# Performance work log

Measured on AMD Instinct MI355X. Metric: run time of the kernel, lower is better.

Reference implementation:

```python
import jax, jax.numpy as jnp
import numpy as np

NUM_USER = 24000
NUM_ITEM = 8000
DIM_E = 64
V_DIM = 2048
T_DIM = 384
TOPK = 10
N_UI_LAYERS = 2
LAMBDA = 0.9
N_INTER = 400000


def _build_sim(x):
    xn = x / jnp.linalg.norm(x, axis=-1, keepdims=True)
    return xn @ xn.T


def _knn_sym(sim, topk):
    # top-k per row -> sparse graph with symmetric (D^-1/2 A D^-1/2) normalization
    n = sim.shape[0]
    val, ind = jax.lax.top_k(sim, topk)            # [n, k]
    row = jnp.repeat(jnp.arange(n), topk)
    w = val.reshape(-1)
    col = ind.reshape(-1)
    deg = jax.ops.segment_sum(w, row, num_segments=n)
    dis = jnp.where(deg > 0, deg ** -0.5, 0.0)     # inf -> 0 as in torch masked_fill
    return col, dis[row] * w * dis[col]


def setup_inputs() -> dict:
    key = jax.random.key(0)
    ks = jax.random.split(key, 12)
    user_emb = jax.random.normal(ks[0], (NUM_USER, DIM_E), jnp.float32) * 0.1
    item_emb = jax.random.normal(ks[1], (NUM_ITEM, DIM_E), jnp.float32) * 0.1
    v_feat = jax.random.normal(ks[2], (NUM_ITEM, V_DIM), jnp.float32)
    t_feat = jax.random.normal(ks[3], (NUM_ITEM, T_DIM), jnp.float32)
    W_v = jax.random.normal(ks[4], (V_DIM, DIM_E), jnp.float32) * (1.0 / np.sqrt(V_DIM))
    b_v = jnp.zeros((DIM_E,), jnp.float32)
    W_t = jax.random.normal(ks[5], (T_DIM, DIM_E), jnp.float32) * (1.0 / np.sqrt(T_DIM))
    b_t = jnp.zeros((DIM_E,), jnp.float32)
    Wq1 = jax.random.normal(ks[6], (DIM_E, DIM_E), jnp.float32) * (1.0 / np.sqrt(DIM_E))
    bq1 = jnp.zeros((DIM_E,), jnp.float32)
    wq2 = jax.random.normal(ks[7], (DIM_E,), jnp.float32) * (1.0 / np.sqrt(DIM_E))
    # bipartite user-item interaction edges, symmetrized (as in __init__)
    u = jax.random.randint(ks[8], (N_INTER,), 0, NUM_USER)
    it = jax.random.randint(ks[9], (N_INTER,), 0, NUM_ITEM) + NUM_USER
    ei = jnp.stack([u, it])
    edge_index = jnp.concatenate([ei, ei[::-1]], axis=1)  # [2, 2*N_INTER]
    # original (frozen) multimodal KNN graphs built from raw features at init
    orig_img_cols, orig_img_w = _knn_sym(_build_sim(v_feat), TOPK)
    orig_txt_cols, orig_txt_w = _knn_sym(_build_sim(t_feat), TOPK)
    return {"user_emb": user_emb, "item_emb": item_emb, "v_feat": v_feat,
            "t_feat": t_feat, "W_v": W_v, "b_v": b_v, "W_t": W_t, "b_t": b_t,
            "Wq1": Wq1, "bq1": bq1, "wq2": wq2,
            "orig_img_w": orig_img_w, "orig_txt_w": orig_txt_w,
            "edge_index": edge_index,
            "orig_img_cols": orig_img_cols, "orig_txt_cols": orig_txt_cols}


def reference(user_emb, item_emb, v_feat, t_feat, W_v, b_v, W_t, b_t,
              Wq1, bq1, wq2, orig_img_w, orig_txt_w,
              edge_index, orig_img_cols, orig_txt_cols):
    n_user, n_item = user_emb.shape[0], item_emb.shape[0]
    # modality projections
    image_feats = v_feat @ W_v + b_v
    text_feats = t_feat @ W_t + b_t
    # fresh KNN graphs from projected features (build_item_graph=True path)
    img_cols, img_w = _knn_sym(_build_sim(image_feats), TOPK)
    txt_cols, txt_w = _knn_sym(_build_sim(text_feats), TOPK)
    row = jnp.repeat(jnp.arange(n_item), TOPK)

    def fused_spmm(cols_new, w_new, cols_orig, w_orig, x):
        # (1-lam)*A_new + lam*A_orig, applied as a single sparse matmul
        rows = jnp.concatenate([row, row])
        cols = jnp.concatenate([cols_new, cols_orig])
        w = jnp.concatenate([(1.0 - LAMBDA) * w_new,
                             LAMBDA * jax.lax.stop_gradient(w_orig)])
        return jax.ops.segment_sum(w[:, None] * x[cols], rows, num_segments=n_item)

    # NOTE: source bug reproduced - mm_layers loop always re-reads item_embedding,
    # so effective propagation depth is 1 regardless of mm_layers.
    image_item = fused_spmm(img_cols, img_w, orig_img_cols, orig_img_w, item_emb)
    text_item = fused_spmm(txt_cols, txt_w, orig_txt_cols, orig_txt_w, item_emb)

    def q(x):
        return jnp.tanh(x @ Wq1 + bq1) @ wq2  # [n_item]

    att = jnp.stack([q(image_item), q(text_item)], axis=-1)  # [n_item, 2]
    wgt = jax.nn.softmax(att, axis=-1)
    h = wgt[:, :1] * image_item + wgt[:, 1:] * text_item

    # user-item GCN propagation with sym degree normalization
    ego = jnp.concatenate([user_emb, item_emb], axis=0)
    n = ego.shape[0]
    r, c = edge_index[0], edge_index[1]
    deg = jax.ops.segment_sum(jnp.ones_like(r, dtype=ego.dtype), r, num_segments=n)
    dis = jnp.where(deg > 0, deg ** -0.5, 0.0)
    norm = dis[r] * dis[c]
    embs = [ego]
    for _ in range(N_UI_LAYERS):
        ego = jax.ops.segment_sum(norm[:, None] * ego[c], r, num_segments=n)
        embs.append(ego)
    all_emb = jnp.mean(jnp.stack(embs, axis=1), axis=1)
    u_g, i_g = all_emb[:n_user], all_emb[n_user:]
    h_norm = h / jnp.maximum(jnp.linalg.norm(h, axis=1, keepdims=True), 1e-12)
    i_g = i_g + h_norm
    return jnp.concatenate([u_g, i_g], axis=0)
```

## Files before the change

### kernel.cpp

```cpp
#include <hip/hip_runtime.h>
#include <math.h>

#define N_USER 24000
#define N_ITEM 8000
#define N_NODE 32000
#define N_EDGE 800000
#define NJC    16
#define JCH    512

typedef __attribute__((ext_vector_type(8))) short bf16x8;
typedef __attribute__((ext_vector_type(4))) float f32x4;

__device__ __forceinline__ float wred_sum(float v) {
#pragma unroll
  for (int off = 32; off; off >>= 1) v += __shfl_xor(v, off, 64);
  return v;
}

__device__ __forceinline__ unsigned short f2bf(float f) {
  unsigned int u = __float_as_uint(f);
  unsigned int r = (u + 0x7fffu + ((u >> 16) & 1u)) >> 16;
  return (unsigned short)r;
}
__device__ __forceinline__ float bf2f(unsigned short h) {
  return __uint_as_float(((unsigned int)h) << 16);
}

__device__ __forceinline__ unsigned int umx(unsigned int a, unsigned int b) { return a > b ? a : b; }
__device__ __forceinline__ unsigned int umn(unsigned int a, unsigned int b) { return a < b ? a : b; }
__device__ __forceinline__ unsigned int umed3(unsigned int a, unsigned int b, unsigned int c) {
  unsigned int d;
  asm("v_med3_u32 %0, %1, %2, %3" : "=v"(d) : "v"(a), "v"(b), "v"(c));
  return d;
}

__device__ __forceinline__ float key_val(unsigned int k) {
  return ((float)(int)(k >> 13) - 131080.0f) * (1.0f / 131072.0f);
}
__device__ __forceinline__ int key_idx(unsigned int k) {
  return 8191 - (int)(k & 8191u);
}

#define NB_G 378
__global__ __launch_bounds__(256) void k_gemm_count(
    const float* __restrict__ Xi, const float* __restrict__ Wi,
    const float* __restrict__ Xt, const float* __restrict__ Wt,
    float* __restrict__ Pi, float* __restrict__ Pt,
    const int* __restrict__ r, int* __restrict__ degi)
{
  __shared__ char lds2[24576];
  char* ldsXH = lds2;
  char* ldsXL = lds2 + 8192;
  char* ldsWH = lds2 + 16384;
  char* ldsWL = lds2 + 20480;
  const int tid = threadIdx.x;
  const int b = blockIdx.x;
  if (b >= NB_G) {
    int e = (b - NB_G) * 256 + tid;
    atomicAdd(&degi[r[e]], 1);
    return;
  }
  const int m0 = (b % 63) * 128;
  const int cy = b / 63;
  const float* X; const float* W; float* out; int K, kc0, ksteps;
  if (cy < 4) { X = Xi; W = Wi; K = 2048; kc0 = cy * 512; ksteps = 16;
                out = Pi + (size_t)cy * N_ITEM * 64; }
  else        { X = Xt; W = Wt; K = 384;  kc0 = (cy - 4) * 192; ksteps = 6;
                out = Pt + (size_t)(cy - 4) * N_ITEM * 64; }
  const int l = tid & 63;
  const int wid = tid >> 6;
  f32x4 acc[2][4] = {};

  for (int ks = 0; ks < ksteps; ++ks) {
    int k0 = kc0 + ks * 32;
    __syncthreads();
#pragma unroll
    for (int lq = 0; lq < 4; ++lq) {
      int u = tid + lq * 256;
      int rr = u >> 3, q = u & 7;
      int grow = m0 + rr; if (grow > N_ITEM - 1) grow = N_ITEM - 1;
      float4 xv = *(const float4*)(X + (size_t)grow * K + k0 + q * 4);
      unsigned short h0 = f2bf(xv.x), h1 = f2bf(xv.y), h2 = f2bf(xv.z), h3 = f2bf(xv.w);
      unsigned int hA = ((unsigned int)h1 << 16) | h0;
      unsigned int hB = ((unsigned int)h3 << 16) | h2;
      unsigned short l0 = f2bf(xv.x - bf2f(h0)), l1 = f2bf(xv.y - bf2f(h1));
      unsigned short l2 = f2bf(xv.z - bf2f(h2)), l3 = f2bf(xv.w - bf2f(h3));
      unsigned int lA = ((unsigned int)l1 << 16) | l0;
      unsigned int lB = ((unsigned int)l3 << 16) | l2;
      int slot = q >> 1;
      int bo = rr * 64 + ((slot ^ ((rr >> 1) & 3)) << 4) + (q & 1) * 8;
      *(int2*)(ldsXH + bo) = make_int2((int)hA, (int)hB);
      *(int2*)(ldsXL + bo) = make_int2((int)lA, (int)lB);
    }
#pragma unroll
    for (int lq = 0; lq < 2; ++lq) {
      int u = tid + lq * 256;
      int kb = u >> 4, nq = (u & 15) * 4;
      float4 wv = *(const float4*)(W + (size_t)(k0 + kb) * 64 + nq);
      int slot = kb >> 3, within = kb & 7;
      float wa[4] = {wv.x, wv.y, wv.z, wv.w};
#pragma unroll
      for (int j = 0; j < 4; ++j) {
        int n = nq + j;
        unsigned short h = f2bf(wa[j]);
        unsigned short lo = f2bf(wa[j] - bf2f(h));
        int bo = n * 64 + ((slot ^ ((n >> 1) & 3)) << 4) + within * 2;
        *(unsigned short*)(ldsWH + bo) = h;
        *(unsigned short*)(ldsWL + bo) = lo;
      }
    }
    __syncthreads();
    bf16x8 xh[2], xl[2], wh[4], wl[4];
    int slot = l >> 4;
#pragma unroll
    for (int s = 0; s < 2; ++s) {
      int rr = wid * 32 + s * 16 + (l & 15);
      int bo = rr * 64 + ((slot ^ ((rr >> 1) & 3)) << 4);
      xh[s] = *(const bf16x8*)(ldsXH + bo);
      xl[s] = *(const bf16x8*)(ldsXL + bo);
    }
#pragma unroll
    for (int nt = 0; nt < 4; ++nt) {
      int n = nt * 16 + (l & 15);
      int bo = n * 64 + ((slot ^ ((n >> 1) & 3)) << 4);
      wh[nt] = *(const bf16x8*)(ldsWH + bo);
      wl[nt] = *(const bf16x8*)(ldsWL + bo);
    }
#pragma unroll
    for (int s = 0; s < 2; ++s)
#pragma unroll
      for (int nt = 0; nt < 4; ++nt) {
        acc[s][nt] = __builtin_amdgcn_mfma_f32_16x16x32_bf16(xh[s], wh[nt], acc[s][nt], 0, 0, 0);
        acc[s][nt] = __builtin_amdgcn_mfma_f32_16x16x32_bf16(xh[s], wl[nt], acc[s][nt], 0, 0, 0);
        acc[s][nt] = __builtin_amdgcn_mfma_f32_16x16x32_bf16(xl[s], wh[nt], acc[s][nt], 0, 0, 0);
      }
  }
#pragma unroll
  for (int s = 0; s < 2; ++s)
#pragma unroll
    for (int nt = 0; nt < 4; ++nt)
#pragma unroll
      for (int r4 = 0; r4 < 4; ++r4) {
        int gi = m0 + wid * 32 + s * 16 + ((l >> 4) << 2) + r4;
        int gn = nt * 16 + (l & 15);
        if (gi < N_ITEM) out[(size_t)gi * 64 + gn] = acc[s][nt][r4];
      }
}

__global__ __launch_bounds__(256) void norm_dual(
    const float* __restrict__ Pi, const float* __restrict__ bi,
    unsigned short* __restrict__ Xhi, unsigned short* __restrict__ Xli,
    const float* __restrict__ Pt, const float* __restrict__ bt,
    unsigned short* __restrict__ Xht, unsigned short* __restrict__ Xlt)
{
  const float* P; const float* bias; unsigned short *Xh, *Xl; int nk;
  if (blockIdx.y == 0) { P = Pi; bias = bi; Xh = Xhi; Xl = Xli; nk = 4; }
  else                 { P = Pt; bias = bt; Xh = Xht; Xl = Xlt; nk = 2; }
  int row = blockIdx.x * 4 + (threadIdx.x >> 6);
  int lane = threadIdx.x & 63;
  size_t o = (size_t)row * 64 + lane;
  float v = bias[lane];
  for (int q = 0; q < nk; ++q) v += P[(size_t)q * N_ITEM * 64 + o];
  float ss = wred_sum(v * v);
  float xn = v * rsqrtf(ss);
  unsigned short hi = f2bf(xn);
  Xh[o] = hi;
  Xl[o] = f2bf(xn - bf2f(hi));
}

#define NB_SIM 2016
__global__ __launch_bounds__(256) void k_sim_scan(
    const unsigned short* __restrict__ Xhi, const unsigned short* __restrict__ Xli,
    const unsigned short* __restrict__ Xht, const unsigned short* __restrict__ Xlt,
    unsigned int* __restrict__ pk,
    const int* __restrict__ degi, int* __restrict__ offs, float* __restrict__ disui)
{
  __shared__ char lds[2 * 2 * 32 * 128];
  const int tid = threadIdx.x;

  if (blockIdx.x == 0) {
    int* stot  = (int*)lds;
    int* sbase = (int*)lds + 512;
    int lane = tid & 63, w = tid >> 6;
    for (int k = 0; k < 125; ++k) {
      int c = w * 125 + k;
      int d = degi[c * 64 + lane];
      int s = d;
#pragma unroll
      for (int off = 32; off; off >>= 1) s += __shfl_xor(s, off, 64);
      if (lane == 0) stot[c] = s;
    }
    __syncthreads();
    if (w == 0) {
      int run = 0;
      for (int r = 0; r < 8; ++r) {
        int idx = r * 64 + lane;
        int v = (idx < 500) ? stot[idx] : 0;
        int p = v;
#pragma unroll
        for (int off = 1; off < 64; off <<= 1) {
          int n = __shfl_up(p, off, 64);
          if (lane >= off) p += n;
        }
        if (idx < 500) sbase[idx] = run + p - v;
        run += __shfl(p, 63, 64);
      }
    }
    __syncthreads();
    for (int k = 0; k < 125; ++k) {
      int c = w * 125 + k;
      int i = c * 64 + lane;
      int d = degi[i];
      int p = d;
#pragma unroll
      for (int off = 1; off < 64; off <<= 1) {
        int n = __shfl_up(p, off, 64);
        if (lane >= off) p += n;
      }
      offs[i] = sbase[c] + p - d;
      disui[i] = d > 0 ? rsqrtf((float)d) : 0.f;
    }
    if (tid == 0) offs[N_NODE] = N_EDGE;
    return;
  }

  const int b = blockIdx.x - 1;
  const int bz = b / 1008;
  const int rem = b % 1008;
  const int by = rem / 63;
  const int bx = rem % 63;
  const unsigned short* Xh = bz ? Xht : Xhi;
  const unsigned short* Xl = bz ? Xlt : Xli;
  unsigned int* pkm = pk + (size_t)bz * N_ITEM * (NJC * 10);

  const int l = tid & 63;
  const int wid = tid >> 6;
  const int ib = bx * 128 + wid * 32;
  const int jc = by * JCH;
  const bool lastc = (jc + JCH > N_ITEM);

  bf16x8 bh[2][2], bl[2][2];
#pragma unroll
  for (int s = 0; s < 2; ++s) {
    int irow = ib + s * 16 + (l & 15);
    if (irow > N_ITEM - 1) irow = N_ITEM - 1;
    int ksl = (l >> 4) * 8;
#pragma unroll
    for (int kh = 0; kh < 2; ++kh) {
      bh[s][kh] = *(const bf16x8*)(Xh + (size_t)irow * 64 + kh * 32 + ksl);
      bl[s][kh] = *(const bf16x8*)(Xl + (size_t)irow * 64 + kh * 32 + ksl);
    }
  }

  unsigned int K0[10], K1[10];
#pragma unroll
  for (int t = 0; t < 10; ++t) { K0[t] = 0u; K1[t] = 0u; }

  auto stage = [&](int bb, int p) {
    int row = tid >> 3, cb = (tid & 7) * 16;
    int gr = jc + p * 32 + row;
    if (gr > N_ITEM - 1) gr = N_ITEM - 1;
    int4 vh = *(const int4*)(Xh + (size_t)gr * 64 + (cb >> 1));
    int4 vl = *(const int4*)(Xl + (size_t)gr * 64 + (cb >> 1));
    int bo = (row * 128 + cb) ^ ((row & 7) << 4);
    *(int4*)(lds + bb * 8192 + bo) = vh;
    *(int4*)(lds + bb * 8192 + 4096 + bo) = vl;
  };

#define EPI(MASKED)                                                            \
  _Pragma("unroll")                                                            \
  for (int s = 0; s < 2; ++s) {                                                \
    unsigned int* K = s ? K1 : K0;                                             \
    _Pragma("unroll")                                                          \
    for (int t = 0; t < 2; ++t) {                                              \
      _Pragma("unroll")                                                        \
      for (int r = 0; r < 4; ++r) {                                            \
        float f = acc[t][s][r];                                                \
        unsigned int v19 = (unsigned int)(int)(f * 131072.0f + 131080.0f);     \
        unsigned int key = (v19 << 13) | (unsigned int)jinv[t * 4 + r];        \
        if (MASKED) key = (jinv[t * 4 + r] >= 192) ? key : 0u;                 \
        _Pragma("unroll")                                                      \
        for (int q = 9; q >= 1; --q) K[q] = umed3(K[q - 1], K[q], key);        \
        K[0] = umx(K[0], key);                                                 \
      }                                                                        \
    }                                                                          \
  }

  stage(0, 0);
  int cur = 0;
  for (int p = 0; p < 16; ++p) {
    __syncthreads();
    if (p < 15) stage(cur ^ 1, p + 1);
    const char* ldsH = lds + cur * 8192;
    const char* ldsL = ldsH + 4096;
    f32x4 acc[2][2] = {};
#pragma unroll
    for (int t = 0; t < 2; ++t) {
      int jr = t * 16 + (l & 15);
      int sw = (jr & 7) << 4;
      int rb = jr * 128 + ((l >> 4) << 4);
      bf16x8 ah0 = *(const bf16x8*)(ldsH + (rb ^ sw));
      bf16x8 ah1 = *(const bf16x8*)(ldsH + ((rb + 64) ^ sw));
      bf16x8 al0 = *(const bf16x8*)(ldsL + (rb ^ sw));
      bf16x8 al1 = *(const bf16x8*)(ldsL + ((rb + 64) ^ sw));
#pragma unroll
      for (int s = 0; s < 2; ++s) {
        acc[t][s] = __builtin_amdgcn_mfma_f32_16x16x32_bf16(ah0, bh[s][0], acc[t][s], 0, 0, 0);
        acc[t][s] = __builtin_amdgcn_mfma_f32_16x16x32_bf16(ah1, bh[s][1], acc[t][s], 0, 0, 0);
        acc[t][s] = __builtin_amdgcn_mfma_f32_16x16x32_bf16(ah0, bl[s][0], acc[t][s], 0, 0, 0);
        acc[t][s] = __builtin_amdgcn_mfma_f32_16x16x32_bf16(ah1, bl[s][1], acc[t][s], 0, 0, 0);
        acc[t][s] = __builtin_amdgcn_mfma_f32_16x16x32_bf16(al0, bh[s][0], acc[t][s], 0, 0, 0);
        acc[t][s] = __builtin_amdgcn_mfma_f32_16x16x32_bf16(al1, bh[s][1], acc[t][s], 0, 0, 0);
      }
    }
    const int jg0 = jc + p * 32 + ((l >> 4) << 2);
    int jinv[8];
#pragma unroll
    for (int t = 0; t < 2; ++t)
#pragma unroll
      for (int r = 0; r < 4; ++r)
        jinv[t * 4 + r] = 8191 - (jg0 + t * 16 + r);
    if (!lastc) { EPI(false) } else { EPI(true) }
    cur ^= 1;
  }
#undef EPI

#pragma unroll
  for (int s = 0; s < 2; ++s) {
    unsigned int* K = s ? K1 : K0;
    unsigned int kv[10];
#pragma unroll
    for (int t = 0; t < 10; ++t) {
      unsigned int m = K[0];
      m = umx(m, (unsigned int)__shfl_xor((int)m, 16, 64));
      m = umx(m, (unsigned int)__shfl_xor((int)m, 32, 64));
      bool own = (K[0] == m);
#pragma unroll
      for (int q2 = 0; q2 < 9; ++q2) K[q2] = own ? K[q2 + 1] : K[q2];
      K[9] = own ? 0u : K[9];
      kv[t] = m;
    }
    int i = ib + s * 16 + (l & 15);
    if (l < 16 && i < N_ITEM) {
      size_t base = ((size_t)i * NJC + by) * 10;
#pragma unroll
      for (int t = 0; t < 10; ++t) pkm[base + t] = kv[t];
    }
  }
}

#define NB_M 4000
__global__ __launch_bounds__(256) void k_merge_fill(
    const unsigned int* __restrict__ pk,
    float* __restrict__ tv_i, int* __restrict__ tc_i, float* __restrict__ dis_i,
    float* __restrict__ tv_t, int* __restrict__ tc_t, float* __restrict__ dis_t,
    const int* __restrict__ r, const int* __restrict__ c,
    const int* __restrict__ offs, int* __restrict__ cursor, int* __restrict__ csr)
{
  int b = blockIdx.x;
  int tid = threadIdx.x;
  if (b >= NB_M) {
    int e = (b - NB_M) * 256 + tid;
    int rr = r[e];
    int pos = offs[rr] + atomicAdd(&cursor[rr], 1);
    csr[pos] = c[e];
    return;
  }
  int my = b / 2000, mx = b % 2000;
  float* tv; int* tc; float* dis;
  if (my == 0) { tv = tv_i; tc = tc_i; dis = dis_i; }
  else         { tv = tv_t; tc = tc_t; dis = dis_t; }
  int lane = tid & 63;
  int row = mx * 4 + (tid >> 6);
  size_t base = (size_t)my * N_ITEM * (NJC * 10) + (size_t)row * (NJC * 10);
  unsigned int k0 = pk[base + lane];
  unsigned int k1 = pk[base + 64 + lane];
  unsigned int k2 = (lane < 32) ? pk[base + 128 + lane] : 0u;
  float deg = 0.f, keepv = 0.f; int keepc = 0;
  for (int t = 0; t < 10; ++t) {
    unsigned int m = umx(umx(k0, k1), k2);
#pragma unroll
    for (int off = 32; off; off >>= 1)
      m = umx(m, (unsigned int)__shfl_xor((int)m, off, 64));
    deg += key_val(m);
    if (k0 == m) k0 = 0u;
    else if (k1 == m) k1 = 0u;
    else if (k2 == m) k2 = 0u;
    if (lane == t) { keepv = key_val(m); keepc = key_idx(m); }
  }
  if (lane < 10) { tv[(size_t)row * 10 + lane] = keepv; tc[(size_t)row * 10 + lane] = keepc; }
  if (lane == 0) dis[row] = deg > 0.f ? rsqrtf(deg) : 0.f;
}

#define NB_S 2000
__global__ __launch_bounds__(256) void k_spmm_prop1(
    const float* __restrict__ tv_i, const int* __restrict__ tc_i, const float* __restrict__ dis_i,
    const float* __restrict__ ow_i, const int* __restrict__ oc_i,
    const float* __restrict__ tv_t, const int* __restrict__ tc_t, const float* __restrict__ dis_t,
    const float* __restrict__ ow_t, const int* __restrict__ oc_t,
    const float* __restrict__ item_emb,
    const float* __restrict__ Wq1, const float* __restrict__ bq1,
    const float* __restrict__ wq2, float* __restrict__ hn,
    const float* __restrict__ ue, float* __restrict__ E1,
    const int* __restrict__ offs, const int* __restrict__ csr,
    const float* __restrict__ dis)
{
  __shared__ float Wlds[64 * 64];
  __shared__ float sm[4][2][64];
  int tid = threadIdx.x;
  int lane = tid & 63, wid = tid >> 6;
  int b = blockIdx.x;
  if (b >= NB_S) {
    int row = (b - NB_S) * 4 + wid;
    int q = lane >> 3, c8 = lane & 7;
    float4 acc0 = make_float4(0.f, 0.f, 0.f, 0.f);
    float4 acc1 = make_float4(0.f, 0.f, 0.f, 0.f);
    int e0 = offs[row], e1 = offs[row + 1];
    for (int e = e0 + q; e < e1; e += 8) {
      int cc = csr[e];
      const float* src = cc < N_USER ? ue + (size_t)cc * 64
                                     : item_emb + (size_t)(cc - N_USER) * 64;
      float4 v0 = *(const float4*)(src + c8 * 8);
      float4 v1 = *(const float4*)(src + c8 * 8 + 4);
      float d = dis[cc];
      acc0.x += d * v0.x; acc0.y += d * v0.y; acc0.z += d * v0.z; acc0.w += d * v0.w;
      acc1.x += d * v1.x; acc1.y += d * v1.y; acc1.z += d * v1.z; acc1.w += d * v1.w;
    }
#pragma unroll
    for (int off = 8; off <= 32; off <<= 1) {
      acc0.x += __shfl_xor(acc0.x, off, 64);
      acc0.y += __shfl_xor(acc0.y, off, 64);
      acc0.z += __shfl_xor(acc0.z, off, 64);
      acc0.w += __shfl_xor(acc0.w, off, 64);
      acc1.x += __shfl_xor(acc1.x, off, 64);
      acc1.y += __shfl_xor(acc1.y, off, 64);
      acc1.z += __shfl_xor(acc1.z, off, 64);
      acc1.w += __shfl_xor(acc1.w, off, 64);
    }
    if (q == 0) {
      float dr = dis[row];
      acc0.x *= dr; acc0.y *= dr; acc0.z *= dr; acc0.w *= dr;
      acc1.x *= dr; acc1.y *= dr; acc1.z *= dr; acc1.w *= dr;
      *(float4*)(E1 + (size_t)row * 64 + c8 * 8) = acc0;
      *(float4*)(E1 + (size_t)row * 64 + c8 * 8 + 4) = acc1;
    }
    return;
  }
  int row = b * 4 + wid;
#pragma unroll
  for (int s = 0; s < 4; ++s) {
    int idx = tid + s * 256;
    ((float4*)Wlds)[idx] = ((const float4*)Wq1)[idx];
  }
  float a0 = 0.f, a1 = 0.f;
  {
    float disr = dis_i[row];
#pragma unroll
    for (int t = 0; t < 10; ++t) {
      int c = tc_i[(size_t)row * 10 + t];
      a0 += 0.1f * disr * tv_i[(size_t)row * 10 + t] * dis_i[c] * item_emb[(size_t)c * 64 + lane];
    }
#pragma unroll
    for (int t = 0; t < 10; ++t) {
      int c = oc_i[(size_t)row * 10 + t];
      a0 += 0.9f * ow_i[(size_t)row * 10 + t] * item_emb[(size_t)c * 64 + lane];
    }
  }
  {
    float disr = dis_t[row];
#pragma unroll
    for (int t = 0; t < 10; ++t) {
      int c = tc_t[(size_t)row * 10 + t];
      a1 += 0.1f * disr * tv_t[(size_t)row * 10 + t] * dis_t[c] * item_emb[(size_t)c * 64 + lane];
    }
#pragma unroll
    for (int t = 0; t < 10; ++t) {
      int c = oc_t[(size_t)row * 10 + t];
      a1 += 0.9f * ow_t[(size_t)row * 10 + t] * item_emb[(size_t)c * 64 + lane];
    }
  }
  sm[wid][0][lane] = a0;
  sm[wid][1][lane] = a1;
  __syncthreads();
  float y0 = bq1[lane], y1 = bq1[lane];
  for (int k = 0; k < 64; ++k) {
    float w = Wlds[k * 64 + lane];
    y0 += sm[wid][0][k] * w;
    y1 += sm[wid][1][k] * w;
  }
  float wq = wq2[lane];
  float s0 = wred_sum(tanhf(y0) * wq);
  float s1 = wred_sum(tanhf(y1) * wq);
  float mx = fmaxf(s0, s1);
  float e0 = expf(s0 - mx), e1 = expf(s1 - mx);
  float inv = 1.f / (e0 + e1);
  float h = (e0 * inv) * a0 + (e1 * inv) * a1;
  float n2 = wred_sum(h * h);
  float nrm = fmaxf(sqrtf(n2), 1e-12f);
  hn[(size_t)row * 64 + lane] = h / nrm;
}

__global__ __launch_bounds__(256) void k_prop2(
    const float* __restrict__ in, const float* __restrict__ ue,
    const float* __restrict__ ie, float* __restrict__ out,
    const int* __restrict__ offs, const int* __restrict__ csr,
    const float* __restrict__ dis, const float* __restrict__ hn)
{
  int tid = threadIdx.x;
  int lane = tid & 63, wid = tid >> 6;
  int row = blockIdx.x * 4 + wid;
  int q = lane >> 3, c8 = lane & 7;
  float4 acc0 = make_float4(0.f, 0.f, 0.f, 0.f);
  float4 acc1 = make_float4(0.f, 0.f, 0.f, 0.f);
  int e0 = offs[row], e1 = offs[row + 1];
  for (int e = e0 + q; e < e1; e += 8) {
    int cc = csr[e];
    const float* src = in + (size_t)cc * 64;
    float4 v0 = *(const float4*)(src + c8 * 8);
    float4 v1 = *(const float4*)(src + c8 * 8 + 4);
    float d = dis[cc];
    acc0.x += d * v0.x; acc0.y += d * v0.y; acc0.z += d * v0.z; acc0.w += d * v0.w;
    acc1.x += d * v1.x; acc1.y += d * v1.y; acc1.z += d * v1.z; acc1.w += d * v1.w;
  }
#pragma unroll
  for (int off = 8; off <= 32; off <<= 1) {
    acc0.x += __shfl_xor(acc0.x, off, 64);
    acc0.y += __shfl_xor(acc0.y, off, 64);
    acc0.z += __shfl_xor(acc0.z, off, 64);
    acc0.w += __shfl_xor(acc0.w, off, 64);
    acc1.x += __shfl_xor(acc1.x, off, 64);
    acc1.y += __shfl_xor(acc1.y, off, 64);
    acc1.z += __shfl_xor(acc1.z, off, 64);
    acc1.w += __shfl_xor(acc1.w, off, 64);
  }
  if (q == 0) {
    float dr = dis[row];
    acc0.x *= dr; acc0.y *= dr; acc0.z *= dr; acc0.w *= dr;
    acc1.x *= dr; acc1.y *= dr; acc1.z *= dr; acc1.w *= dr;
    const float* egop = (row < N_USER) ? ue + (size_t)row * 64
                                       : ie + (size_t)(row - N_USER) * 64;
    float4 eg0 = *(const float4*)(egop + c8 * 8);
    float4 eg1 = *(const float4*)(egop + c8 * 8 + 4);
    float4 l10 = *(const float4*)(in + (size_t)row * 64 + c8 * 8);
    float4 l11 = *(const float4*)(in + (size_t)row * 64 + c8 * 8 + 4);
    float4 o0, o1;
    o0.x = (eg0.x + l10.x + acc0.x) * (1.f / 3.f);
    o0.y = (eg0.y + l10.y + acc0.y) * (1.f / 3.f);
    o0.z = (eg0.z + l10.z + acc0.z) * (1.f / 3.f);
    o0.w = (eg0.w + l10.w + acc0.w) * (1.f / 3.f);
    o1.x = (eg1.x + l11.x + acc1.x) * (1.f / 3.f);
    o1.y = (eg1.y + l11.y + acc1.y) * (1.f / 3.f);
    o1.z = (eg1.z + l11.z + acc1.z) * (1.f / 3.f);
    o1.w = (eg1.w + l11.w + acc1.w) * (1.f / 3.f);
    if (row >= N_USER) {
      const float* hp = hn + (size_t)(row - N_USER) * 64;
      float4 h0 = *(const float4*)(hp + c8 * 8);
      float4 h1 = *(const float4*)(hp + c8 * 8 + 4);
      o0.x += h0.x; o0.y += h0.y; o0.z += h0.z; o0.w += h0.w;
      o1.x += h1.x; o1.y += h1.y; o1.z += h1.z; o1.w += h1.w;
    }
    *(float4*)(out + (size_t)row * 64 + c8 * 8) = o0;
    *(float4*)(out + (size_t)row * 64 + c8 * 8 + 4) = o1;
  }
}

extern "C" void kernel_launch(void* const* d_in, const int* in_sizes, int n_in,
                              void* d_out, int out_size, void* d_ws, size_t ws_size,
                              hipStream_t stream)
{
  (void)in_sizes; (void)n_in; (void)out_size; (void)ws_size;
  const float* user_emb = (const float*)d_in[0];
  const float* item_emb = (const float*)d_in[1];
  const float* v_feat   = (const float*)d_in[2];
  const float* t_feat   = (const float*)d_in[3];
  const float* W_v      = (const float*)d_in[4];
  const float* b_v      = (const float*)d_in[5];
  const float* W_t      = (const float*)d_in[6];
  const float* b_t      = (const float*)d_in[7];
  const float* Wq1      = (const float*)d_in[8];
  const float* bq1      = (const float*)d_in[9];
  const float* wq2      = (const float*)d_in[10];
  const float* ow_i     = (const float*)d_in[11];
  const float* ow_t     = (const float*)d_in[12];
  const int*   eidx     = (const int*)d_in[13];
  const int*   oc_i     = (const int*)d_in[14];
  const int*   oc_t     = (const int*)d_in[15];
  float* out = (float*)d_out;

  char* wp = (char*)d_ws;
  auto alloc = [&](size_t bytes) -> void* {
    void* p = (void*)wp;
    wp += (bytes + 255) & ~(size_t)255;
    return p;
  };
  char* regionA = (char*)alloc((size_t)8 * N_ITEM * 64 * 4 + 1024);
  char* regionB = (char*)alloc((size_t)N_NODE * 64 * 4 + 1024);
  float* Pp_i = (float*)regionA;
  float* Pp_t = (float*)regionB;
  unsigned int* pk = (unsigned int*)regionA;
  float* E1 = (float*)regionB;

  unsigned short* Xhi = (unsigned short*)alloc((size_t)N_ITEM * 64 * 2);
  unsigned short* Xli = (unsigned short*)alloc((size_t)N_ITEM * 64 * 2);
  unsigned short* Xht = (unsigned short*)alloc((size_t)N_ITEM * 64 * 2);
  unsigned short* Xlt = (unsigned short*)alloc((size_t)N_ITEM * 64 * 2);
  float* tv_i  = (float*)alloc((size_t)N_ITEM * 10 * 4);
  int*   tc_i  = (int*)  alloc((size_t)N_ITEM * 10 * 4);
  float* dis_i = (float*)alloc((size_t)N_ITEM * 4);
  float* tv_t  = (float*)alloc((size_t)N_ITEM * 10 * 4);
  int*   tc_t  = (int*)  alloc((size_t)N_ITEM * 10 * 4);
  float* dis_t = (float*)alloc((size_t)N_ITEM * 4);
  float* hn    = (float*)alloc((size_t)N_ITEM * 64 * 4);
  int*   degcur= (int*)  alloc((size_t)2 * N_NODE * 4);
  int*   degi  = degcur;
  int*   curs  = degcur + N_NODE;
  int*   offs  = (int*)  alloc((size_t)(N_NODE + 1) * 4);
  float* disui = (float*)alloc((size_t)N_NODE * 4);
  int*   csr   = (int*)  alloc((size_t)N_EDGE * 4);

  hipMemsetAsync(degcur, 0, (size_t)2 * N_NODE * 4, stream);
  k_gemm_count<<<NB_G + 3125, 256, 0, stream>>>(v_feat, W_v, t_feat, W_t, Pp_i, Pp_t,
                                                eidx, degi);
  norm_dual<<<dim3(2000, 2), 256, 0, stream>>>(Pp_i, b_v, Xhi, Xli, Pp_t, b_t, Xht, Xlt);
  k_sim_scan<<<NB_SIM + 1, 256, 0, stream>>>(Xhi, Xli, Xht, Xlt, pk, degi, offs, disui);
  k_merge_fill<<<NB_M + 3125, 256, 0, stream>>>(pk, tv_i, tc_i, dis_i, tv_t, tc_t, dis_t,
                                                eidx, eidx + N_EDGE, offs, curs, csr);
  k_spmm_prop1<<<NB_S + 8000, 256, 0, stream>>>(tv_i, tc_i, dis_i, ow_i, oc_i,
                                                tv_t, tc_t, dis_t, ow_t, oc_t,
                                                item_emb, Wq1, bq1, wq2, hn,
                                                user_emb, E1, offs, csr, disui);
  k_prop2<<<8000, 256, 0, stream>>>(E1, user_emb, item_emb, out, offs, csr, disui, hn);
}
```

Measured before the change: 301.0 us.

## Double similarity-scan block size so each staged column tile serves more rows

The similarity top-k kernel moves from 256 to 512 threads per block, with each block covering 256 item rows instead of 128. The grid shrinks from 2016 to 1024 scan blocks, and each thread stages half as many bytes (int2 instead of int4) into the shared LDS tile. The aim is to reuse each staged column chunk across twice as many rows, cutting redundant global loads of the column features. The trade-offs are fewer blocks for occupancy, 8-byte LDS writes, and a rebalanced prefix-scan block, which now uses 8 waves with bounds checks.

Result: no change. 305.3 us (+1.4%).

```diff
diff --git a/kernel.cpp b/kernel.cpp
--- a/kernel.cpp
+++ b/kernel.cpp
@@ -168,8 +168,8 @@
   Xl[o] = f2bf(xn - bf2f(hi));
 }
 
-#define NB_SIM 2016
-__global__ __launch_bounds__(256) void k_sim_scan(
+#define NB_SIM 1024
+__global__ __launch_bounds__(512) void k_sim_scan(
     const unsigned short* __restrict__ Xhi, const unsigned short* __restrict__ Xli,
     const unsigned short* __restrict__ Xht, const unsigned short* __restrict__ Xlt,
     unsigned int* __restrict__ pk,
@@ -177,65 +177,68 @@
 {
   __shared__ char lds[2 * 2 * 32 * 128];
   const int tid = threadIdx.x;
+  const int l = tid & 63;
+  const int wid = tid >> 6;
 
   if (blockIdx.x == 0) {
     int* stot  = (int*)lds;
     int* sbase = (int*)lds + 512;
-    int lane = tid & 63, w = tid >> 6;
-    for (int k = 0; k < 125; ++k) {
-      int c = w * 125 + k;
-      int d = degi[c * 64 + lane];
-      int s = d;
-#pragma unroll
-      for (int off = 32; off; off >>= 1) s += __shfl_xor(s, off, 64);
-      if (lane == 0) stot[c] = s;
+    for (int k = 0; k < 63; ++k) {
+      int c = wid * 63 + k;
+      if (c < 500) {
+        int d = degi[c * 64 + l];
+        int s = d;
+#pragma unroll
+        for (int off = 32; off; off >>= 1) s += __shfl_xor(s, off, 64);
+        if (l == 0) stot[c] = s;
+      }
     }
     __syncthreads();
-    if (w == 0) {
+    if (wid == 0) {
       int run = 0;
       for (int r = 0; r < 8; ++r) {
-        int idx = r * 64 + lane;
+        int idx = r * 64 + l;
         int v = (idx < 500) ? stot[idx] : 0;
         int p = v;
 #pragma unroll
         for (int off = 1; off < 64; off <<= 1) {
           int n = __shfl_up(p, off, 64);
-          if (lane >= off) p += n;
+          if (l >= off) p += n;
         }
         if (idx < 500) sbase[idx] = run + p - v;
         run += __shfl(p, 63, 64);
       }
     }
     __syncthreads();
-    for (int k = 0; k < 125; ++k) {
-      int c = w * 125 + k;
-      int i = c * 64 + lane;
-      int d = degi[i];
-      int p = d;
-#pragma unroll
-      for (int off = 1; off < 64; off <<= 1) {
-        int n = __shfl_up(p, off, 64);
-        if (lane >= off) p += n;
+    for (int k = 0; k < 63; ++k) {
+      int c = wid * 63 + k;
+      if (c < 500) {
+        int i = c * 64 + l;
+        int d = degi[i];
+        int p = d;
+#pragma unroll
+        for (int off = 1; off < 64; off <<= 1) {
+          int n = __shfl_up(p, off, 64);
+          if (l >= off) p += n;
+        }
+        offs[i] = sbase[c] + p - d;
+        disui[i] = d > 0 ? rsqrtf((float)d) : 0.f;
       }
-      offs[i] = sbase[c] + p - d;
-      disui[i] = d > 0 ? rsqrtf((float)d) : 0.f;
     }
     if (tid == 0) offs[N_NODE] = N_EDGE;
     return;
   }
 
   const int b = blockIdx.x - 1;
-  const int bz = b / 1008;
-  const int rem = b % 1008;
-  const int by = rem / 63;
-  const int bx = rem % 63;
+  const int bz = b >> 9;
+  const int rem = b & 511;
+  const int by = rem >> 5;
+  const int bx = rem & 31;
   const unsigned short* Xh = bz ? Xht : Xhi;
   const unsigned short* Xl = bz ? Xlt : Xli;
   unsigned int* pkm = pk + (size_t)bz * N_ITEM * (NJC * 10);
 
-  const int l = tid & 63;
-  const int wid = tid >> 6;
-  const int ib = bx * 128 + wid * 32;
+  const int ib = bx * 256 + wid * 32;
   const int jc = by * JCH;
   const bool lastc = (jc + JCH > N_ITEM);
 
@@ -257,14 +260,14 @@
   for (int t = 0; t < 10; ++t) { K0[t] = 0u; K1[t] = 0u; }
 
   auto stage = [&](int bb, int p) {
-    int row = tid >> 3, cb = (tid & 7) * 16;
+    int row = tid >> 4, cb = (tid & 15) * 8;
     int gr = jc + p * 32 + row;
     if (gr > N_ITEM - 1) gr = N_ITEM - 1;
-    int4 vh = *(const int4*)(Xh + (size_t)gr * 64 + (cb >> 1));
-    int4 vl = *(const int4*)(Xl + (size_t)gr * 64 + (cb >> 1));
+    int2 vh = *(const int2*)(Xh + (size_t)gr * 64 + (cb >> 1));
+    int2 vl = *(const int2*)(Xl + (size_t)gr * 64 + (cb >> 1));
     int bo = (row * 128 + cb) ^ ((row & 7) << 4);
-    *(int4*)(lds + bb * 8192 + bo) = vh;
-    *(int4*)(lds + bb * 8192 + 4096 + bo) = vl;
+    *(int2*)(lds + bb * 8192 + bo) = vh;
+    *(int2*)(lds + bb * 8192 + 4096 + bo) = vl;
   };
 
 #define EPI(MASKED)                                                            \
@@ -622,7 +625,7 @@
   k_gemm_count<<<NB_G + 3125, 256, 0, stream>>>(v_feat, W_v, t_feat, W_t, Pp_i, Pp_t,
                                                 eidx, degi);
   norm_dual<<<dim3(2000, 2), 256, 0, stream>>>(Pp_i, b_v, Xhi, Xli, Pp_t, b_t, Xht, Xlt);
-  k_sim_scan<<<NB_SIM + 1, 256, 0, stream>>>(Xhi, Xli, Xht, Xlt, pk, degi, offs, disui);
+  k_sim_scan<<<NB_SIM + 1, 512, 0, stream>>>(Xhi, Xli, Xht, Xlt, pk, degi, offs, disui);
   k_merge_fill<<<NB_M + 3125, 256, 0, stream>>>(pk, tv_i, tc_i, dis_i, tv_t, tc_t, dis_t,
                                                 eidx, eidx + N_EDGE, offs, curs, csr);
   k_spmm_prop1<<<NB_S + 8000, 256, 0, stream>>>(tv_i, tc_i, dis_i, ow_i, oc_i,
```

## Rebalance kernel fusion: move scan, CSR fill and propagation layers to earlier kernels

Applied to the files above, without the earlier changes.

Re-partitions work across kernels. The degree scan now runs with the normalization kernel, the CSR fill is co-scheduled with the similarity top-k scan, and layer-1 propagation runs alongside the merge. User-row layer-2 propagation runs alongside the multimodal spmm, leaving only item rows for the final kernel. The similarity kernel now uses 512-thread blocks covering 256 rows with narrower staging loads, which halves its grid. The aim is to fill idle CUs during tail-heavy phases, at the cost of new data dependencies across stages that must stay ordered.

After: 375.3 us. 24.7% more time.

```diff
diff --git a/kernel.cpp b/kernel.cpp
--- a/kernel.cpp
+++ b/kernel.cpp
@@ -147,17 +147,66 @@
       }
 }
 
-__global__ __launch_bounds__(256) void norm_dual(
+__global__ __launch_bounds__(256) void k_norm_scan(
     const float* __restrict__ Pi, const float* __restrict__ bi,
     unsigned short* __restrict__ Xhi, unsigned short* __restrict__ Xli,
     const float* __restrict__ Pt, const float* __restrict__ bt,
-    unsigned short* __restrict__ Xht, unsigned short* __restrict__ Xlt)
+    unsigned short* __restrict__ Xht, unsigned short* __restrict__ Xlt,
+    const int* __restrict__ degi, int* __restrict__ offs, float* __restrict__ disui)
 {
-  const float* P; const float* bias; unsigned short *Xh, *Xl; int nk;
-  if (blockIdx.y == 0) { P = Pi; bias = bi; Xh = Xhi; Xl = Xli; nk = 4; }
-  else                 { P = Pt; bias = bt; Xh = Xht; Xl = Xlt; nk = 2; }
-  int row = blockIdx.x * 4 + (threadIdx.x >> 6);
-  int lane = threadIdx.x & 63;
+  __shared__ int sbuf[1024];
+  const int tid = threadIdx.x;
+  if (blockIdx.x == 0) {
+    int* stot  = sbuf;
+    int* sbase = sbuf + 512;
+    int lane = tid & 63, w = tid >> 6;
+    for (int k = 0; k < 125; ++k) {
+      int c = w * 125 + k;
+      int d = degi[c * 64 + lane];
+      int s = d;
+#pragma unroll
+      for (int off = 32; off; off >>= 1) s += __shfl_xor(s, off, 64);
+      if (lane == 0) stot[c] = s;
+    }
+    __syncthreads();
+    if (w == 0) {
+      int run = 0;
+      for (int r = 0; r < 8; ++r) {
+        int idx = r * 64 + lane;
+        int v = (idx < 500) ? stot[idx] : 0;
+        int p = v;
+#pragma unroll
+        for (int off = 1; off < 64; off <<= 1) {
+          int n = __shfl_up(p, off, 64);
+          if (lane >= off) p += n;
+        }
+        if (idx < 500) sbase[idx] = run + p - v;
+        run += __shfl(p, 63, 64);
+      }
+    }
+    __syncthreads();
+    for (int k = 0; k < 125; ++k) {
+      int c = w * 125 + k;
+      int i = c * 64 + lane;
+      int d = degi[i];
+      int p = d;
+#pragma unroll
+      for (int off = 1; off < 64; off <<= 1) {
+        int n = __shfl_up(p, off, 64);
+        if (lane >= off) p += n;
+      }
+      offs[i] = sbase[c] + p - d;
+      disui[i] = d > 0 ? rsqrtf((float)d) : 0.f;
+    }
+    if (tid == 0) offs[N_NODE] = N_EDGE;
+    return;
+  }
+  int b = blockIdx.x - 1;
+  const float* P; const float* bias; unsigned short *Xh, *Xl; int nk; int mx;
+  if (b < 2000) { P = Pi; bias = bi; Xh = Xhi; Xl = Xli; nk = 4; mx = b; }
+  else          { P = Pt; bias = bt; Xh = Xht; Xl = Xlt; nk = 2; mx = b - 2000; }
+  int row = mx * 4 + (tid >> 6);
+  int lane = tid & 63;
   size_t o = (size_t)row * 64 + lane;
   float v = bias[lane];
   for (int q = 0; q < nk; ++q) v += P[(size_t)q * N_ITEM * 64 + o];
@@ -168,74 +217,40 @@
   Xl[o] = f2bf(xn - bf2f(hi));
 }
 
-#define NB_SIM 2016
-__global__ __launch_bounds__(256) void k_sim_scan(
+#define NB_SIM 1024
+#define NB_FILL 1563
+__global__ __launch_bounds__(512) void k_sim_fill(
     const unsigned short* __restrict__ Xhi, const unsigned short* __restrict__ Xli,
     const unsigned short* __restrict__ Xht, const unsigned short* __restrict__ Xlt,
     unsigned int* __restrict__ pk,
-    const int* __restrict__ degi, int* __restrict__ offs, float* __restrict__ disui)
+    const int* __restrict__ r, const int* __restrict__ c,
+    const int* __restrict__ offs, int* __restrict__ cursor, int* __restrict__ csr)
 {
   __shared__ char lds[2 * 2 * 32 * 128];
   const int tid = threadIdx.x;
-
-  if (blockIdx.x == 0) {
-    int* stot  = (int*)lds;
-    int* sbase = (int*)lds + 512;
-    int lane = tid & 63, w = tid >> 6;
-    for (int k = 0; k < 125; ++k) {
-      int c = w * 125 + k;
-      int d = degi[c * 64 + lane];
-      int s = d;
-#pragma unroll
-      for (int off = 32; off; off >>= 1) s += __shfl_xor(s, off, 64);
-      if (lane == 0) stot[c] = s;
-    }
-    __syncthreads();
-    if (w == 0) {
-      int run = 0;
-      for (int r = 0; r < 8; ++r) {
-        int idx = r * 64 + lane;
-        int v = (idx < 500) ? stot[idx] : 0;
-        int p = v;
-#pragma unroll
-        for (int off = 1; off < 64; off <<= 1) {
-          int n = __shfl_up(p, off, 64);
-          if (lane >= off) p += n;
-        }
-        if (idx < 500) sbase[idx] = run + p - v;
-        run += __shfl(p, 63, 64);
-      }
-    }
-    __syncthreads();
-    for (int k = 0; k < 125; ++k) {
-      int c = w * 125 + k;
-      int i = c * 64 + lane;
-      int d = degi[i];
-      int p = d;
-#pragma unroll
-      for (int off = 1; off < 64; off <<= 1) {
-        int n = __shfl_up(p, off, 64);
-        if (lane >= off) p += n;
-      }
-      offs[i] = sbase[c] + p - d;
-      disui[i] = d > 0 ? rsqrtf((float)d) : 0.f;
-    }
-    if (tid == 0) offs[N_NODE] = N_EDGE;
+  const int l = tid & 63;
+  const int wid = tid >> 6;
+
+  if (blockIdx.x >= NB_SIM) {
+    int e = (blockIdx.x - NB_SIM) * 512 + tid;
+    if (e < N_EDGE) {
+      int rr = r[e];
+      int pos = offs[rr] + atomicAdd(&cursor[rr], 1);
+      csr[pos] = c[e];
+    }
     return;
   }
 
-  const int b = blockIdx.x - 1;
-  const int bz = b / 1008;
-  const int rem = b % 1008;
-  const int by = rem / 63;
-  const int bx = rem % 63;
+  const int b = blockIdx.x;
+  const int bz = b >> 9;
+  const int rem = b & 511;
+  const int by = rem >> 5;
+  const int bx = rem & 31;
   const unsigned short* Xh = bz ? Xht : Xhi;
   const unsigned short* Xl = bz ? Xlt : Xli;
   unsigned int* pkm = pk + (size_t)bz * N_ITEM * (NJC * 10);
 
-  const int l = tid & 63;
-  const int wid = tid >> 6;
-  const int ib = bx * 128 + wid * 32;
+  const int ib = bx * 256 + wid * 32;
   const int jc = by * JCH;
   const bool lastc = (jc + JCH > N_ITEM);
 
@@ -257,14 +272,14 @@
   for (int t = 0; t < 10; ++t) { K0[t] = 0u; K1[t] = 0u; }
 
   auto stage = [&](int bb, int p) {
-    int row = tid >> 3, cb = (tid & 7) * 16;
+    int row = tid >> 4, cb = (tid & 15) * 8;
     int gr = jc + p * 32 + row;
     if (gr > N_ITEM - 1) gr = N_ITEM - 1;
-    int4 vh = *(const int4*)(Xh + (size_t)gr * 64 + (cb >> 1));
-    int4 vl = *(const int4*)(Xl + (size_t)gr * 64 + (cb >> 1));
+    int2 vh = *(const int2*)(Xh + (size_t)gr * 64 + (cb >> 1));
+    int2 vl = *(const int2*)(Xl + (size_t)gr * 64 + (cb >> 1));
     int bo = (row * 128 + cb) ^ ((row & 7) << 4);
-    *(int4*)(lds + bb * 8192 + bo) = vh;
-    *(int4*)(lds + bb * 8192 + 4096 + bo) = vl;
+    *(int2*)(lds + bb * 8192 + bo) = vh;
+    *(int2*)(lds + bb * 8192 + 4096 + bo) = vl;
   };
 
 #define EPI(MASKED)                                                            \
@@ -274,11 +289,11 @@
     _Pragma("unroll")                                                          \
     for (int t = 0; t < 2; ++t) {                                              \
       _Pragma("unroll")                                                        \
-      for (int r = 0; r < 4; ++r) {                                            \
-        float f = acc[t][s][r];                                                \
+      for (int r2 = 0; r2 < 4; ++r2) {                                         \
+        float f = acc[t][s][r2];                                               \
         unsigned int v19 = (unsigned int)(int)(f * 131072.0f + 131080.0f);     \
-        unsigned int key = (v19 << 13) | (unsigned int)jinv[t * 4 + r];        \
-        if (MASKED) key = (jinv[t * 4 + r] >= 192) ? key : 0u;                 \
+        unsigned int key = (v19 << 13) | (unsigned int)jinv[t * 4 + r2];       \
+        if (MASKED) key = (jinv[t * 4 + r2] >= 192) ? key : 0u;                \
         _Pragma("unroll")                                                      \
         for (int q = 9; q >= 1; --q) K[q] = umed3(K[q - 1], K[q], key);        \
         K[0] = umx(K[0], key);                                                 \
@@ -318,8 +333,8 @@
 #pragma unroll
     for (int t = 0; t < 2; ++t)
 #pragma unroll
-      for (int r = 0; r < 4; ++r)
-        jinv[t * 4 + r] = 8191 - (jg0 + t * 16 + r);
+      for (int r2 = 0; r2 < 4; ++r2)
+        jinv[t * 4 + r2] = 8191 - (jg0 + t * 16 + r2);
     if (!lastc) { EPI(false) } else { EPI(true) }
     cur ^= 1;
   }
@@ -350,28 +365,59 @@
 }
 
 #define NB_M 4000
-__global__ __launch_bounds__(256) void k_merge_fill(
+__global__ __launch_bounds__(256) void k_merge_prop1(
     const unsigned int* __restrict__ pk,
     float* __restrict__ tv_i, int* __restrict__ tc_i, float* __restrict__ dis_i,
     float* __restrict__ tv_t, int* __restrict__ tc_t, float* __restrict__ dis_t,
-    const int* __restrict__ r, const int* __restrict__ c,
-    const int* __restrict__ offs, int* __restrict__ cursor, int* __restrict__ csr)
+    const float* __restrict__ ue, const float* __restrict__ ie,
+    float* __restrict__ E1,
+    const int* __restrict__ offs, const int* __restrict__ csr,
+    const float* __restrict__ dis)
 {
   int b = blockIdx.x;
   int tid = threadIdx.x;
+  int lane = tid & 63, wid = tid >> 6;
   if (b >= NB_M) {
-    int e = (b - NB_M) * 256 + tid;
-    int rr = r[e];
-    int pos = offs[rr] + atomicAdd(&cursor[rr], 1);
-    csr[pos] = c[e];
+    int row = (b - NB_M) * 4 + wid;
+    int q = lane >> 3, c8 = lane & 7;
+    float4 acc0 = make_float4(0.f, 0.f, 0.f, 0.f);
+    float4 acc1 = make_float4(0.f, 0.f, 0.f, 0.f);
+    int e0 = offs[row], e1 = offs[row + 1];
+    for (int e = e0 + q; e < e1; e += 8) {
+      int cc = csr[e];
+      const float* src = cc < N_USER ? ue + (size_t)cc * 64
+                                     : ie + (size_t)(cc - N_USER) * 64;
+      float4 v0 = *(const float4*)(src + c8 * 8);
+      float4 v1 = *(const float4*)(src + c8 * 8 + 4);
+      float d = dis[cc];
+      acc0.x += d * v0.x; acc0.y += d * v0.y; acc0.z += d * v0.z; acc0.w += d * v0.w;
+      acc1.x += d * v1.x; acc1.y += d * v1.y; acc1.z += d * v1.z; acc1.w += d * v1.w;
+    }
+#pragma unroll
+    for (int off = 8; off <= 32; off <<= 1) {
+      acc0.x += __shfl_xor(acc0.x, off, 64);
+      acc0.y += __shfl_xor(acc0.y, off, 64);
+      acc0.z += __shfl_xor(acc0.z, off, 64);
+      acc0.w += __shfl_xor(acc0.w, off, 64);
+      acc1.x += __shfl_xor(acc1.x, off, 64);
+      acc1.y += __shfl_xor(acc1.y, off, 64);
+      acc1.z += __shfl_xor(acc1.z, off, 64);
+      acc1.w += __shfl_xor(acc1.w, off, 64);
+    }
+    if (q == 0) {
+      float dr = dis[row];
+      acc0.x *= dr; acc0.y *= dr; acc0.z *= dr; acc0.w *= dr;
+      acc1.x *= dr; acc1.y *= dr; acc1.z *= dr; acc1.w *= dr;
+      *(float4*)(E1 + (size_t)row * 64 + c8 * 8) = acc0;
+      *(float4*)(E1 + (size_t)row * 64 + c8 * 8 + 4) = acc1;
+    }
     return;
   }
   int my = b / 2000, mx = b % 2000;
-  float* tv; int* tc; float* dis;
-  if (my == 0) { tv = tv_i; tc = tc_i; dis = dis_i; }
-  else         { tv = tv_t; tc = tc_t; dis = dis_t; }
-  int lane = tid & 63;
-  int row = mx * 4 + (tid >> 6);
+  float* tv; int* tc; float* dis_m;
+  if (my == 0) { tv = tv_i; tc = tc_i; dis_m = dis_i; }
+  else         { tv = tv_t; tc = tc_t; dis_m = dis_t; }
+  int row = mx * 4 + wid;
   size_t base = (size_t)my * N_ITEM * (NJC * 10) + (size_t)row * (NJC * 10);
   unsigned int k0 = pk[base + lane];
   unsigned int k1 = pk[base + 64 + lane];
@@ -389,11 +435,11 @@
     if (lane == t) { keepv = key_val(m); keepc = key_idx(m); }
   }
   if (lane < 10) { tv[(size_t)row * 10 + lane] = keepv; tc[(size_t)row * 10 + lane] = keepc; }
-  if (lane == 0) dis[row] = deg > 0.f ? rsqrtf(deg) : 0.f;
+  if (lane == 0) dis_m[row] = deg > 0.f ? rsqrtf(deg) : 0.f;
 }
 
 #define NB_S 2000
-__global__ __launch_bounds__(256) void k_spmm_prop1(
+__global__ __launch_bounds__(256) void k_spmm_prop2u(
     const float* __restrict__ tv_i, const int* __restrict__ tc_i, const float* __restrict__ dis_i,
     const float* __restrict__ ow_i, const int* __restrict__ oc_i,
     const float* __restrict__ tv_t, const int* __restrict__ tc_t, const float* __restrict__ dis_t,
@@ -401,7 +447,8 @@
     const float* __restrict__ item_emb,
     const float* __restrict__ Wq1, const float* __restrict__ bq1,
     const float* __restrict__ wq2, float* __restrict__ hn,
-    const float* __restrict__ ue, float* __restrict__ E1,
+    const float* __restrict__ E1, const float* __restrict__ ue,
+    float* __restrict__ out,
     const int* __restrict__ offs, const int* __restrict__ csr,
     const float* __restrict__ dis)
 {
@@ -418,8 +465,7 @@
     int e0 = offs[row], e1 = offs[row + 1];
     for (int e = e0 + q; e < e1; e += 8) {
       int cc = csr[e];
-      const float* src = cc < N_USER ? ue + (size_t)cc * 64
-                                     : item_emb + (size_t)(cc - N_USER) * 64;
+      const float* src = E1 + (size_t)cc * 64;
       float4 v0 = *(const float4*)(src + c8 * 8);
       float4 v1 = *(const float4*)(src + c8 * 8 + 4);
       float d = dis[cc];
@@ -439,10 +485,21 @@
     }
     if (q == 0) {
       float dr = dis[row];
-      acc0.x *= dr; acc0.y *= dr; acc0.z *= dr; acc0.w *= dr;
-      acc1.x *= dr; acc1.y *= dr; acc1.z *= dr; acc1.w *= dr;
-      *(float4*)(E1 + (size_t)row * 64 + c8 * 8) = acc0;
-      *(float4*)(E1 + (size_t)row * 64 + c8 * 8 + 4) = acc1;
+      float4 eg0 = *(const float4*)(ue + (size_t)row * 64 + c8 * 8);
+      float4 eg1 = *(const float4*)(ue + (size_t)row * 64 + c8 * 8 + 4);
+      float4 l10 = *(const float4*)(E1 + (size_t)row * 64 + c8 * 8);
+      float4 l11 = *(const float4*)(E1 + (size_t)row * 64 + c8 * 8 + 4);
+      float4 o0, o1;
+      o0.x = (eg0.x + l10.x + dr * acc0.x) * (1.f / 3.f);
+      o0.y = (eg0.y + l10.y + dr * acc0.y) * (1.f / 3.f);
+      o0.z = (eg0.z + l10.z + dr * acc0.z) * (1.f / 3.f);
+      o0.w = (eg0.w + l10.w + dr * acc0.w) * (1.f / 3.f);
+      o1.x = (eg1.x + l11.x + dr * acc1.x) * (1.f / 3.f);
+      o1.y = (eg1.y + l11.y + dr * acc1.y) * (1.f / 3.f);
+      o1.z = (eg1.z + l11.z + dr * acc1.z) * (1.f / 3.f);
+      o1.w = (eg1.w + l11.w + dr * acc1.w) * (1.f / 3.f);
+      *(float4*)(out + (size_t)row * 64 + c8 * 8) = o0;
+      *(float4*)(out + (size_t)row * 64 + c8 * 8 + 4) = o1;
     }
     return;
   }
@@ -500,15 +557,15 @@
   hn[(size_t)row * 64 + lane] = h / nrm;
 }
 
-__global__ __launch_bounds__(256) void k_prop2(
-    const float* __restrict__ in, const float* __restrict__ ue,
-    const float* __restrict__ ie, float* __restrict__ out,
+__global__ __launch_bounds__(256) void k_prop2i(
+    const float* __restrict__ in, const float* __restrict__ ie,
+    float* __restrict__ out,
     const int* __restrict__ offs, const int* __restrict__ csr,
     const float* __restrict__ dis, const float* __restrict__ hn)
 {
   int tid = threadIdx.x;
   int lane = tid & 63, wid = tid >> 6;
-  int row = blockIdx.x * 4 + wid;
+  int row = N_USER + blockIdx.x * 4 + wid;
   int q = lane >> 3, c8 = lane & 7;
   float4 acc0 = make_float4(0.f, 0.f, 0.f, 0.f);
   float4 acc1 = make_float4(0.f, 0.f, 0.f, 0.f);
@@ -535,30 +592,22 @@
   }
   if (q == 0) {
     float dr = dis[row];
-    acc0.x *= dr; acc0.y *= dr; acc0.z *= dr; acc0.w *= dr;
-    acc1.x *= dr; acc1.y *= dr; acc1.z *= dr; acc1.w *= dr;
-    const float* egop = (row < N_USER) ? ue + (size_t)row * 64
-                                       : ie + (size_t)(row - N_USER) * 64;
-    float4 eg0 = *(const float4*)(egop + c8 * 8);
-    float4 eg1 = *(const float4*)(egop + c8 * 8 + 4);
+    int irow = row - N_USER;
+    float4 eg0 = *(const float4*)(ie + (size_t)irow * 64 + c8 * 8);
+    float4 eg1 = *(const float4*)(ie + (size_t)irow * 64 + c8 * 8 + 4);
     float4 l10 = *(const float4*)(in + (size_t)row * 64 + c8 * 8);
     float4 l11 = *(const float4*)(in + (size_t)row * 64 + c8 * 8 + 4);
+    float4 h0 = *(const float4*)(hn + (size_t)irow * 64 + c8 * 8);
+    float4 h1 = *(const float4*)(hn + (size_t)irow * 64 + c8 * 8 + 4);
     float4 o0, o1;
-    o0.x = (eg0.x + l10.x + acc0.x) * (1.f / 3.f);
-    o0.y = (eg0.y + l10.y + acc0.y) * (1.f / 3.f);
-    o0.z = (eg0.z + l10.z + acc0.z) * (1.f / 3.f);
-    o0.w = (eg0.w + l10.w + acc0.w) * (1.f / 3.f);
-    o1.x = (eg1.x + l11.x + acc1.x) * (1.f / 3.f);
-    o1.y = (eg1.y + l11.y + acc1.y) * (1.f / 3.f);
-    o1.z = (eg1.z + l11.z + acc1.z) * (1.f / 3.f);
-    o1.w = (eg1.w + l11.w + acc1.w) * (1.f / 3.f);
-    if (row >= N_USER) {
-      const float* hp = hn + (size_t)(row - N_USER) * 64;
-      float4 h0 = *(const float4*)(hp + c8 * 8);
-      float4 h1 = *(const float4*)(hp + c8 * 8 + 4);
-      o0.x += h0.x; o0.y += h0.y; o0.z += h0.z; o0.w += h0.w;
-      o1.x += h1.x; o1.y += h1.y; o1.z += h1.z; o1.w += h1.w;
-    }
+    o0.x = (eg0.x + l10.x + dr * acc0.x) * (1.f / 3.f) + h0.x;
+    o0.y = (eg0.y + l10.y + dr * acc0.y) * (1.f / 3.f) + h0.y;
+    o0.z = (eg0.z + l10.z + dr * acc0.z) * (1.f / 3.f) + h0.z;
+    o0.w = (eg0.w + l10.w + dr * acc0.w) * (1.f / 3.f) + h0.w;
+    o1.x = (eg1.x + l11.x + dr * acc1.x) * (1.f / 3.f) + h1.x;
+    o1.y = (eg1.y + l11.y + dr * acc1.y) * (1.f / 3.f) + h1.y;
+    o1.z = (eg1.z + l11.z + dr * acc1.z) * (1.f / 3.f) + h1.z;
+    o1.w = (eg1.w + l11.w + dr * acc1.w) * (1.f / 3.f) + h1.w;
     *(float4*)(out + (size_t)row * 64 + c8 * 8) = o0;
     *(float4*)(out + (size_t)row * 64 + c8 * 8 + 4) = o1;
   }
@@ -593,7 +642,8 @@
     wp += (bytes + 255) & ~(size_t)255;
     return p;
   };
-  char* regionA = (char*)alloc((size_t)8 * N_ITEM * 64 * 4 + 1024);
+  size_t pk_bytes = (size_t)2 * N_ITEM * (NJC * 10) * 4;
+  char* regionA = (char*)alloc(pk_bytes + 1024);
   char* regionB = (char*)alloc((size_t)N_NODE * 64 * 4 + 1024);
   float* Pp_i = (float*)regionA;
   float* Pp_t = (float*)regionB;
@@ -621,13 +671,15 @@
   hipMemsetAsync(degcur, 0, (size_t)2 * N_NODE * 4, stream);
   k_gemm_count<<<NB_G + 3125, 256, 0, stream>>>(v_feat, W_v, t_feat, W_t, Pp_i, Pp_t,
                                                 eidx, degi);
-  norm_dual<<<dim3(2000, 2), 256, 0, stream>>>(Pp_i, b_v, Xhi, Xli, Pp_t, b_t, Xht, Xlt);
-  k_sim_scan<<<NB_SIM + 1, 256, 0, stream>>>(Xhi, Xli, Xht, Xlt, pk, degi, offs, disui);
-  k_merge_fill<<<NB_M + 3125, 256, 0, stream>>>(pk, tv_i, tc_i, dis_i, tv_t, tc_t, dis_t,
-                                                eidx, eidx + N_EDGE, offs, curs, csr);
-  k_spmm_prop1<<<NB_S + 8000, 256, 0, stream>>>(tv_i, tc_i, dis_i, ow_i, oc_i,
-                                                tv_t, tc_t, dis_t, ow_t, oc_t,
-                                                item_emb, Wq1, bq1, wq2, hn,
-                                                user_emb, E1, offs, csr, disui);
-  k_prop2<<<8000, 256, 0, stream>>>(E1, user_emb, item_emb, out, offs, csr, disui, hn);
-}
+  k_norm_scan<<<4001, 256, 0, stream>>>(Pp_i, b_v, Xhi, Xli, Pp_t, b_t, Xht, Xlt,
+                                        degi, offs, disui);
+  k_sim_fill<<<NB_SIM + NB_FILL, 512, 0, stream>>>(Xhi, Xli, Xht, Xlt, pk,
+                                                   eidx, eidx + N_EDGE, offs, curs, csr);
+  k_merge_prop1<<<NB_M + 8000, 256, 0, stream>>>(pk, tv_i, tc_i, dis_i, tv_t, tc_t, dis_t,
+                                                 user_emb, item_emb, E1, offs, csr, disui);
+  k_spmm_prop2u<<<NB_S + 6000, 256, 0, stream>>>(tv_i, tc_i, dis_i, ow_i, oc_i,
+                                                 tv_t, tc_t, dis_t, ow_t, oc_t,
+                                                 item_emb, Wq1, bq1, wq2, hn,
+                                                 E1, user_emb, out, offs, csr, disui);
+  k_prop2i<<<2000, 256, 0, stream>>>(E1, item_emb, out, offs, csr, disui, hn);
+}
```
